# Kernel tuning notes

Hardware: AMD Instinct MI355X
Metric: run time of the kernel (lower is better)

Reference implementation:

```python
import jax, jax.numpy as jnp
import numpy as np

ENDING = False  # ending=False -> 'outgoing' triangle update; True -> 'incoming'
EPS = 1e-5


def _ln(x, w, b):
    m = jnp.mean(x, axis=-1, keepdims=True)
    v = jnp.mean((x - m) ** 2, axis=-1, keepdims=True)
    return (x - m) * jax.lax.rsqrt(v + EPS) * w + b


def setup_inputs() -> dict:
    key = jax.random.key(0)
    ks = jax.random.split(key, 6)
    B, N, D = 1, 384, 128
    s = 0.02
    return {
        "x": jax.random.normal(ks[0], (B, N, N, D), jnp.float32),
        "norm_in_w": jnp.ones((D,), jnp.float32),
        "norm_in_b": jnp.zeros((D,), jnp.float32),
        "w_g_in": jax.random.normal(ks[1], (2 * D, D), jnp.float32) * s,
        "w_p_in": jax.random.normal(ks[2], (2 * D, D), jnp.float32) * s,
        "w_g_out": jax.random.normal(ks[3], (D, D), jnp.float32) * s,
        "norm_out_w": jnp.ones((D,), jnp.float32),
        "norm_out_b": jnp.zeros((D,), jnp.float32),
        "w_p_out": jax.random.normal(ks[4], (D, D), jnp.float32) * s,
    }


def reference(x, norm_in_w, norm_in_b, w_g_in, w_p_in, w_g_out,
              norm_out_w, norm_out_b, w_p_out):
    D = x.shape[-1]
    xn = _ln(x, norm_in_w, norm_in_b)                       # [B,N,N,D]
    g_in = jax.nn.sigmoid(jnp.einsum('bijd,ed->bije', xn, w_g_in))  # [B,N,N,2D]
    p = jnp.einsum('bijd,ed->bije', xn, w_p_in) * g_in      # [B,N,N,2D]
    a, b = p[..., :D], p[..., D:]
    if ENDING:
        # incoming: out[i,j,d] = sum_k a[k,i,d] * b[k,j,d]
        t = jnp.einsum('bkid,bkjd->bijd', a, b)
    else:
        # outgoing: out[i,j,d] = sum_k a[i,k,d] * b[j,k,d]
        t = jnp.einsum('bikd,bjkd->bijd', a, b)
    g_out = jax.nn.sigmoid(jnp.einsum('bijd,ed->bije', xn, w_g_out))  # [B,N,N,D]
    return g_out * jnp.einsum('bijd,ed->bije', _ln(t, norm_out_w, norm_out_b), w_p_out)
```

## Files before the change

kernel.cpp:

```cpp
#include <hip/hip_runtime.h>
#include <hip/hip_bf16.h>
#include <math.h>

#define NPOS 147456
#define NSEQ 384

typedef __attribute__((ext_vector_type(4))) float f32x4;
typedef __attribute__((ext_vector_type(8))) short bf16x8;
typedef __attribute__((ext_vector_type(4))) short s16x4;

__device__ __forceinline__ unsigned short f2bf(float f){
  union { float f; unsigned u; } v; v.f = f;
  unsigned r = v.u + 0x7FFFu + ((v.u >> 16) & 1u);
  return (unsigned short)(r >> 16);
}
__device__ __forceinline__ float bf2f(unsigned short h){
  union { unsigned u; float f; } v; v.u = ((unsigned)h) << 16;
  return v.f;
}
__device__ __forceinline__ float fastsig(float x){
  return __builtin_amdgcn_rcpf(1.0f + __expf(-x));
}
__device__ __forceinline__ unsigned pk2(float lo, float hi){
  return (unsigned)f2bf(lo) | ((unsigned)f2bf(hi) << 16);
}
__device__ __forceinline__ void gl16(const unsigned short* g, unsigned short* l){
  __builtin_amdgcn_global_load_lds(
      (const __attribute__((address_space(1))) void*)g,
      (__attribute__((address_space(3))) void*)l, 16, 0, 0);
}

__global__ void wswz_all(const float* __restrict__ wgi, const float* __restrict__ wpi,
                         const float* __restrict__ wgo, const float* __restrict__ wpo,
                         unsigned short* __restrict__ wgi_s, unsigned short* __restrict__ wpi_s,
                         unsigned short* __restrict__ wgo_s, unsigned short* __restrict__ wpo_s){
  int i = blockIdx.x * 256 + threadIdx.x;
  int t = i >> 11;
  int r = i & 2047;
  const float* src; unsigned short* dst; int lt;
  if (t < 16)      { src = wgi; dst = wgi_s; lt = t;      }
  else if (t < 32) { src = wpi; dst = wpi_s; lt = t - 16; }
  else if (t < 40) { src = wgo; dst = wgo_s; lt = t - 32; }
  else             { src = wpo; dst = wpo_s; lt = t - 40; }
  int j = r & 7, lane = (r >> 3) & 63, kk = (r >> 9) & 3;
  int lrow = lane & 15, khh = lane >> 4;
  dst[lt*2048 + r] = f2bf(src[(lt*16 + lrow)*128 + kk*32 + khh*8 + j]);
}

__global__ __launch_bounds__(256, 4) void k1_ln_proj(
    const float* __restrict__ x,
    const float* __restrict__ ln_w, const float* __restrict__ ln_b,
    const unsigned short* __restrict__ wg_sw,
    const unsigned short* __restrict__ wp_sw,
    const unsigned short* __restrict__ wgo_sw,
    unsigned short* __restrict__ a_t,
    unsigned short* __restrict__ b_t,
    unsigned short* __restrict__ g_t)
{
  __shared__ unsigned short xn[128][128];
  unsigned short* wbuf = &xn[0][0];
  unsigned short* obuf = wbuf + 8192;

  const int tid  = threadIdx.x;
  const int posb = blockIdx.x * 128;
  const int lane = tid & 63;
  const int wid  = tid >> 6;

  const int rql = tid >> 2;
  const int q   = tid & 3;
  #pragma unroll
  for (int rr = 0; rr < 2; ++rr){
    int row = rr*64 + rql;
    const float* xr = x + (size_t)(posb + row) * 128 + q * 32;
    float v[32]; float s = 0.f, s2 = 0.f;
    #pragma unroll
    for (int j2 = 0; j2 < 8; ++j2){
      f32x4 t4 = *(const f32x4*)(xr + j2*4);
      #pragma unroll
      for (int m = 0; m < 4; ++m){ float f = t4[m]; v[j2*4+m] = f; s += f; s2 += f*f; }
    }
    s  += __shfl_xor(s, 1);  s  += __shfl_xor(s, 2);
    s2 += __shfl_xor(s2, 1); s2 += __shfl_xor(s2, 2);
    float mean = s * (1.f/128.f);
    float rstd = rsqrtf(s2 * (1.f/128.f) - mean*mean + 1e-5f);
    int sw = (row & 7) * 8;
    #pragma unroll
    for (int c = 0; c < 4; ++c){
      float n[8];
      #pragma unroll
      for (int j2 = 0; j2 < 8; ++j2){
        int k = q*32 + c*8 + j2;
        n[j2] = (v[c*8+j2] - mean) * rstd * ln_w[k] + ln_b[k];
      }
      uint4 u;
      u.x = pk2(n[0], n[1]); u.y = pk2(n[2], n[3]);
      u.z = pk2(n[4], n[5]); u.w = pk2(n[6], n[7]);
      *(uint4*)&xn[row][(q*32 + c*8) ^ sw] = u;
    }
  }
  __syncthreads();

  const int lrow = lane & 15, kh = lane >> 4;
  bf16x8 afrag[2][4];
  #pragma unroll
  for (int r = 0; r < 2; ++r){
    int row = wid*32 + r*16 + lrow;
    int sw = (row & 7) * 8;
    #pragma unroll
    for (int kk = 0; kk < 4; ++kk)
      afrag[r][kk] = *(const bf16x8*)&xn[row][(kk*32 + kh*8) ^ sw];
  }
  __syncthreads();

  const int kh4 = kh * 4;
  const int scl = wid*4 + kh;
  const int spo = lrow * 8;
  const int wl8 = wid*512 + lane*8;

#define STAGE_PAIR(et, b) do { \
    gl16(wg_sw + (size_t)(et)*2048 + wl8, wbuf + (2*(b)+0)*2048 + wid*512); \
    gl16(wp_sw + (size_t)(et)*2048 + wl8, wbuf + (2*(b)+1)*2048 + wid*512); \
  } while(0)
#define STAGE_G(et, b) do { \
    gl16(wgo_sw + (size_t)(et)*2048 + wl8, wbuf + (b)*2048 + wid*512); \
  } while(0)

  STAGE_PAIR(0, 0);
  __syncthreads();

  for (int et = 0; et < 16; ++et){
    const int b = et & 1;
    const unsigned short* wG = wbuf + (2*b+0)*2048 + lane*8;
    const unsigned short* wP = wbuf + (2*b+1)*2048 + lane*8;
    f32x4 accg0 = {0.f,0.f,0.f,0.f}, accg1 = {0.f,0.f,0.f,0.f};
    f32x4 accp0 = {0.f,0.f,0.f,0.f}, accp1 = {0.f,0.f,0.f,0.f};
    #pragma unroll
    for (int kk = 0; kk < 4; ++kk){
      bf16x8 G = *(const bf16x8*)(wG + kk*512);
      bf16x8 P = *(const bf16x8*)(wP + kk*512);
      accg0 = __builtin_amdgcn_mfma_f32_16x16x32_bf16(afrag[0][kk], G, accg0, 0, 0, 0);
      accg1 = __builtin_amdgcn_mfma_f32_16x16x32_bf16(afrag[1][kk], G, accg1, 0, 0, 0);
      accp0 = __builtin_amdgcn_mfma_f32_16x16x32_bf16(afrag[0][kk], P, accp0, 0, 0, 0);
      accp1 = __builtin_amdgcn_mfma_f32_16x16x32_bf16(afrag[1][kk], P, accp1, 0, 0, 0);
    }
    {
      uint2 u0, u1;
      u0.x = pk2(fastsig(accg0[0])*accp0[0], fastsig(accg0[1])*accp0[1]);
      u0.y = pk2(fastsig(accg0[2])*accp0[2], fastsig(accg0[3])*accp0[3]);
      u1.x = pk2(fastsig(accg1[0])*accp1[0], fastsig(accg1[1])*accp1[1]);
      u1.y = pk2(fastsig(accg1[2])*accp1[2], fastsig(accg1[3])*accp1[3]);
      *(uint2*)&obuf[b*2176 + lrow*136 + wid*32 + kh4]      = u0;
      *(uint2*)&obuf[b*2176 + lrow*136 + wid*32 + 16 + kh4] = u1;
    }
    if (et < 15) STAGE_PAIR(et+1, b^1);
    else         STAGE_G(0, 0);
    __syncthreads();
    {
      bf16x8 vv = *(const bf16x8*)&obuf[b*2176 + scl*136 + spo];
      int colg = et*16 + scl;
      unsigned short* dst = (et < 8) ? (a_t + (size_t)colg * NPOS)
                                     : (b_t + (size_t)(colg - 128) * NPOS);
      *(bf16x8*)(dst + posb + spo) = vv;
    }
  }

  for (int gt = 0; gt < 8; ++gt){
    const int b = gt & 1;
    const unsigned short* wQ = wbuf + b*2048 + lane*8;
    f32x4 a0 = {0.f,0.f,0.f,0.f}, a1 = {0.f,0.f,0.f,0.f};
    #pragma unroll
    for (int kk = 0; kk < 4; ++kk){
      bf16x8 Q = *(const bf16x8*)(wQ + kk*512);
      a0 = __builtin_amdgcn_mfma_f32_16x16x32_bf16(afrag[0][kk], Q, a0, 0, 0, 0);
      a1 = __builtin_amdgcn_mfma_f32_16x16x32_bf16(afrag[1][kk], Q, a1, 0, 0, 0);
    }
    {
      uint2 u0, u1;
      u0.x = pk2(fastsig(a0[0]), fastsig(a0[1]));
      u0.y = pk2(fastsig(a0[2]), fastsig(a0[3]));
      u1.x = pk2(fastsig(a1[0]), fastsig(a1[1]));
      u1.y = pk2(fastsig(a1[2]), fastsig(a1[3]));
      *(uint2*)&obuf[b*2176 + lrow*136 + wid*32 + kh4]      = u0;
      *(uint2*)&obuf[b*2176 + lrow*136 + wid*32 + 16 + kh4] = u1;
    }
    if (gt < 7) STAGE_G(gt+1, b^1);
    __syncthreads();
    {
      bf16x8 vv = *(const bf16x8*)&obuf[b*2176 + scl*136 + spo];
      *(bf16x8*)(g_t + (size_t)(gt*16 + scl) * NPOS + posb + spo) = vv;
    }
  }
#undef STAGE_PAIR
#undef STAGE_G
}

#define K2PAD 56
__global__ __launch_bounds__(256) void k2_tri(
    const unsigned short* __restrict__ a_t,
    const unsigned short* __restrict__ b_t,
    unsigned short* __restrict__ t_t)
{
  __shared__ unsigned short As[128][K2PAD];
  __shared__ unsigned short Bs[128][K2PAD];

  const int d  = blockIdx.z;
  const int i0 = blockIdx.y * 128;
  const int j0 = blockIdx.x * 128;
  const unsigned short* Ab = a_t + (size_t)d * NPOS;
  const unsigned short* Bb = b_t + (size_t)d * NPOS;

  const int tid = threadIdx.x;
  const int wid = tid >> 6, lane = tid & 63;
  const int wr = wid >> 1, wc = wid & 1;
  const int lrow = lane & 15, kh = (lane >> 4) * 8;

  f32x4 acc[4][4];
  #pragma unroll
  for (int r = 0; r < 4; ++r)
    #pragma unroll
    for (int c = 0; c < 4; ++c)
      acc[r][c] = (f32x4){0.f,0.f,0.f,0.f};

  const int sr = tid >> 1, sc = (tid & 1) * 16;

  for (int k0 = 0; k0 < NSEQ; k0 += 32){
    bf16x8 va0 = *(const bf16x8*)(Ab + (size_t)(i0 + sr) * NSEQ + k0 + sc);
    bf16x8 va1 = *(const bf16x8*)(Ab + (size_t)(i0 + sr) * NSEQ + k0 + sc + 8);
    bf16x8 vb0 = *(const bf16x8*)(Bb + (size_t)(j0 + sr) * NSEQ + k0 + sc);
    bf16x8 vb1 = *(const bf16x8*)(Bb + (size_t)(j0 + sr) * NSEQ + k0 + sc + 8);
    __syncthreads();
    *(bf16x8*)&As[sr][sc]     = va0;
    *(bf16x8*)&As[sr][sc + 8] = va1;
    *(bf16x8*)&Bs[sr][sc]     = vb0;
    *(bf16x8*)&Bs[sr][sc + 8] = vb1;
    __syncthreads();

    bf16x8 af[4], bfr[4];
    #pragma unroll
    for (int r = 0; r < 4; ++r)
      af[r] = *(const bf16x8*)&As[wr*64 + r*16 + lrow][kh];
    #pragma unroll
    for (int c = 0; c < 4; ++c)
      bfr[c] = *(const bf16x8*)&Bs[wc*64 + c*16 + lrow][kh];
    #pragma unroll
    for (int r = 0; r < 4; ++r)
      #pragma unroll
      for (int c = 0; c < 4; ++c)
        acc[r][c] = __builtin_amdgcn_mfma_f32_16x16x32_bf16(af[r], bfr[c], acc[r][c], 0, 0, 0);
  }

  unsigned short* Tb = t_t + (size_t)d * NPOS;
  #pragma unroll
  for (int r = 0; r < 4; ++r){
    int i = i0 + wr*64 + r*16 + (lane >> 4) * 4;
    #pragma unroll
    for (int c = 0; c < 4; ++c){
      int j = j0 + wc*64 + c*16 + lrow;
      #pragma unroll
      for (int jj = 0; jj < 4; ++jj)
        Tb[(size_t)(i + jj) * NSEQ + j] = f2bf(acc[r][c][jj]);
    }
  }
}

#define LNS 136
__global__ __launch_bounds__(256, 3) void k3_out(
    const unsigned short* __restrict__ t_t,
    const unsigned short* __restrict__ g_t,
    const float* __restrict__ ln_w, const float* __restrict__ ln_b,
    const unsigned short* __restrict__ wpo_sw,
    float* __restrict__ out)
{
  __shared__ unsigned short traw[128][136];
  __shared__ float regB[9024];
  __shared__ float smean[128], srs[128];

  const int tid = threadIdx.x;
  const int p0  = blockIdx.x * 128;
  const int lane = tid & 63, wid = tid >> 6;

  float* pps = regB;
  float* ppq = regB + 2048;
  unsigned short* lnt = (unsigned short*)regB;
  float (*ltile)[68] = (float(*)[68])regB;

  {
    int d = tid >> 1, c0 = (tid & 1) * 64;
    const unsigned short* src = t_t + (size_t)d * NPOS + p0 + c0;
    #pragma unroll
    for (int j = 0; j < 8; ++j)
      *(bf16x8*)&traw[d][c0 + j*8] = *(const bf16x8*)(src + j*8);
  }
  __syncthreads();

  const int pg = tid & 15, dh = tid >> 4;
  {
    float s8[8] = {0,0,0,0,0,0,0,0}, q8[8] = {0,0,0,0,0,0,0,0};
    #pragma unroll
    for (int jd = 0; jd < 8; ++jd){
      bf16x8 v = *(const bf16x8*)&traw[dh*8 + jd][pg*8];
      #pragma unroll
      for (int p = 0; p < 8; ++p){
        float f = bf2f((unsigned short)v[p]);
        s8[p] += f; q8[p] += f*f;
      }
    }
    #pragma unroll
    for (int p = 0; p < 8; ++p){
      pps[dh*128 + pg*8 + p] = s8[p];
      ppq[dh*128 + pg*8 + p] = q8[p];
    }
  }
  __syncthreads();
  if (tid < 128){
    float s = 0.f, q = 0.f;
    #pragma unroll
    for (int k = 0; k < 16; ++k){ s += pps[k*128 + tid]; q += ppq[k*128 + tid]; }
    float m = s * (1.f/128.f);
    smean[tid] = m;
    srs[tid]   = rsqrtf(q * (1.f/128.f) - m*m + 1e-5f);
  }
  __syncthreads();

  {
    float vv[8][8];
    #pragma unroll
    for (int jd = 0; jd < 8; ++jd){
      bf16x8 v = *(const bf16x8*)&traw[dh*8 + jd][pg*8];
      float w = ln_w[dh*8 + jd], bb = ln_b[dh*8 + jd];
      #pragma unroll
      for (int p = 0; p < 8; ++p)
        vv[jd][p] = (bf2f((unsigned short)v[p]) - smean[pg*8+p]) * srs[pg*8+p] * w + bb;
    }
    #pragma unroll
    for (int p = 0; p < 8; ++p){
      uint4 u;
      u.x = pk2(vv[0][p], vv[1][p]); u.y = pk2(vv[2][p], vv[3][p]);
      u.z = pk2(vv[4][p], vv[5][p]); u.w = pk2(vv[6][p], vv[7][p]);
      *(uint4*)&lnt[(size_t)(pg*8 + p)*LNS + dh*8] = u;
    }
  }
  __syncthreads();

  const int lrow = lane & 15, kh = (lane >> 4) * 8;
  bf16x8 af[2][4];
  #pragma unroll
  for (int r = 0; r < 2; ++r)
    #pragma unroll
    for (int kk = 0; kk < 4; ++kk)
      af[r][kk] = *(const bf16x8*)&lnt[(size_t)(wid*32 + r*16 + lrow)*LNS + kk*32 + kh];
  __syncthreads();

  {
    int e = tid >> 1, c0 = (tid & 1) * 64;
    const unsigned short* src = g_t + (size_t)e * NPOS + p0 + c0;
    #pragma unroll
    for (int j = 0; j < 8; ++j)
      *(bf16x8*)&traw[e][c0 + j*8] = *(const bf16x8*)(src + j*8);
  }
  __syncthreads();

  #pragma unroll
  for (int half = 0; half < 2; ++half){
    #pragma unroll
    for (int cf4 = 0; cf4 < 4; ++cf4){
      int cf = half*4 + cf4;
      const unsigned short* wq = wpo_sw + (size_t)cf*2048 + lane*8;
      bf16x8 bfr[4];
      #pragma unroll
      for (int kk = 0; kk < 4; ++kk)
        bfr[kk] = *(const bf16x8*)(wq + kk*512);
      f32x4 a0 = {0.f,0.f,0.f,0.f}, a1 = {0.f,0.f,0.f,0.f};
      #pragma unroll
      for (int kk = 0; kk < 4; ++kk){
        a0 = __builtin_amdgcn_mfma_f32_16x16x32_bf16(af[0][kk], bfr[kk], a0, 0, 0, 0);
        a1 = __builtin_amdgcn_mfma_f32_16x16x32_bf16(af[1][kk], bfr[kk], a1, 0, 0, 0);
      }
      int e = cf*16 + lrow;
      #pragma unroll
      for (int r = 0; r < 2; ++r){
        f32x4 av = r ? a1 : a0;
        int prow = wid*32 + r*16 + (lane >> 4)*4;
        #pragma unroll
        for (int jj = 0; jj < 4; ++jj){
          float g = bf2f(traw[e][prow + jj]);
          ltile[prow + jj][cf4*16 + lrow] = g * av[jj];
        }
      }
    }
    __syncthreads();
    {
      int pos = tid >> 1, he = tid & 1;
      const float* srcp = &ltile[pos][he*32];
      float* dst = out + (size_t)(p0 + pos)*128 + half*64 + he*32;
      #pragma unroll
      for (int j = 0; j < 8; ++j)
        *(f32x4*)(dst + j*4) = *(const f32x4*)(srcp + j*4);
    }
    __syncthreads();
  }
}

extern "C" void kernel_launch(void* const* d_in, const int* in_sizes, int n_in,
                              void* d_out, int out_size, void* d_ws, size_t ws_size,
                              hipStream_t stream) {
  (void)in_sizes; (void)n_in; (void)out_size; (void)ws_size;
  const float* x   = (const float*)d_in[0];
  const float* niw = (const float*)d_in[1];
  const float* nib = (const float*)d_in[2];
  const float* wgi = (const float*)d_in[3];
  const float* wpi = (const float*)d_in[4];
  const float* wgo = (const float*)d_in[5];
  const float* now = (const float*)d_in[6];
  const float* nob = (const float*)d_in[7];
  const float* wpo = (const float*)d_in[8];
  float* out = (float*)d_out;

  unsigned short* a_t   = (unsigned short*)d_ws;
  unsigned short* b_t   = a_t + (size_t)128 * NPOS;
  unsigned short* g_t   = b_t + (size_t)128 * NPOS;
  unsigned short* t_t   = g_t + (size_t)128 * NPOS;
  unsigned short* wgi_s = t_t + (size_t)128 * NPOS;
  unsigned short* wpi_s = wgi_s + 256 * 128;
  unsigned short* wgo_s = wpi_s + 256 * 128;
  unsigned short* wpo_s = wgo_s + 128 * 128;

  wswz_all<<<384, 256, 0, stream>>>(wgi, wpi, wgo, wpo, wgi_s, wpi_s, wgo_s, wpo_s);

  k1_ln_proj<<<NPOS/128, 256, 0, stream>>>(x, niw, nib, wgi_s, wpi_s, wgo_s, a_t, b_t, g_t);

  dim3 g2(3, 3, 128);
  k2_tri<<<g2, 256, 0, stream>>>(a_t, b_t, t_t);

  k3_out<<<NPOS/128, 256, 0, stream>>>(t_t, g_t, now, nob, wpo_s, out);
}
```

Baseline: 169.0 us.

## Load projection weights directly from global memory and use per-wave output staging

Drops the LDS double-buffered weight staging (global_load_lds) and its block-wide barriers in the projection kernel. Weight fragments are now read straight from global/L2 by each wave, and each wave transposes its own output tile in a private LDS region, so no __syncthreads is needed per tile. This removes 24 block barriers per block at the cost of redundant per-wave global weight reads that rely on cache hits. The within-wave LDS write-then-read relies on wave-level ordering without an explicit barrier.

```diff
diff --git a/kernel.cpp b/kernel.cpp
--- a/kernel.cpp
+++ b/kernel.cpp
@@ -23,11 +23,6 @@
 }
 __device__ __forceinline__ unsigned pk2(float lo, float hi){
   return (unsigned)f2bf(lo) | ((unsigned)f2bf(hi) << 16);
-}
-__device__ __forceinline__ void gl16(const unsigned short* g, unsigned short* l){
-  __builtin_amdgcn_global_load_lds(
-      (const __attribute__((address_space(1))) void*)g,
-      (__attribute__((address_space(3))) void*)l, 16, 0, 0);
 }
 
 __global__ void wswz_all(const float* __restrict__ wgi, const float* __restrict__ wpi,
@@ -58,8 +53,7 @@
     unsigned short* __restrict__ g_t)
 {
   __shared__ unsigned short xn[128][128];
-  unsigned short* wbuf = &xn[0][0];
-  unsigned short* obuf = wbuf + 8192;
+  unsigned short* obase = &xn[0][0];
 
   const int tid  = threadIdx.x;
   const int posb = blockIdx.x * 128;
@@ -112,26 +106,15 @@
   }
   __syncthreads();
 
+  unsigned short* ob = obase + wid * 640;
   const int kh4 = kh * 4;
-  const int scl = wid*4 + kh;
-  const int spo = lrow * 8;
-  const int wl8 = wid*512 + lane*8;
-
-#define STAGE_PAIR(et, b) do { \
-    gl16(wg_sw + (size_t)(et)*2048 + wl8, wbuf + (2*(b)+0)*2048 + wid*512); \
-    gl16(wp_sw + (size_t)(et)*2048 + wl8, wbuf + (2*(b)+1)*2048 + wid*512); \
-  } while(0)
-#define STAGE_G(et, b) do { \
-    gl16(wgo_sw + (size_t)(et)*2048 + wl8, wbuf + (b)*2048 + wid*512); \
-  } while(0)
-
-  STAGE_PAIR(0, 0);
-  __syncthreads();
+  const int och = lane >> 2;
+  const int opo = (lane & 3) * 8;
+  const size_t posw = (size_t)posb + wid*32;
 
   for (int et = 0; et < 16; ++et){
-    const int b = et & 1;
-    const unsigned short* wG = wbuf + (2*b+0)*2048 + lane*8;
-    const unsigned short* wP = wbuf + (2*b+1)*2048 + lane*8;
+    const unsigned short* wG = wg_sw + (size_t)et*2048 + lane*8;
+    const unsigned short* wP = wp_sw + (size_t)et*2048 + lane*8;
     f32x4 accg0 = {0.f,0.f,0.f,0.f}, accg1 = {0.f,0.f,0.f,0.f};
     f32x4 accp0 = {0.f,0.f,0.f,0.f}, accp1 = {0.f,0.f,0.f,0.f};
     #pragma unroll
@@ -149,24 +132,20 @@
       u0.y = pk2(fastsig(accg0[2])*accp0[2], fastsig(accg0[3])*accp0[3]);
       u1.x = pk2(fastsig(accg1[0])*accp1[0], fastsig(accg1[1])*accp1[1]);
       u1.y = pk2(fastsig(accg1[2])*accp1[2], fastsig(accg1[3])*accp1[3]);
-      *(uint2*)&obuf[b*2176 + lrow*136 + wid*32 + kh4]      = u0;
-      *(uint2*)&obuf[b*2176 + lrow*136 + wid*32 + 16 + kh4] = u1;
-    }
-    if (et < 15) STAGE_PAIR(et+1, b^1);
-    else         STAGE_G(0, 0);
-    __syncthreads();
+      *(uint2*)&ob[lrow*40 + kh4]      = u0;
+      *(uint2*)&ob[lrow*40 + 16 + kh4] = u1;
+    }
     {
-      bf16x8 vv = *(const bf16x8*)&obuf[b*2176 + scl*136 + spo];
-      int colg = et*16 + scl;
+      bf16x8 vv = *(const bf16x8*)&ob[och*40 + opo];
+      int colg = et*16 + och;
       unsigned short* dst = (et < 8) ? (a_t + (size_t)colg * NPOS)
                                      : (b_t + (size_t)(colg - 128) * NPOS);
-      *(bf16x8*)(dst + posb + spo) = vv;
+      *(bf16x8*)(dst + posw + opo) = vv;
     }
   }
 
   for (int gt = 0; gt < 8; ++gt){
-    const int b = gt & 1;
-    const unsigned short* wQ = wbuf + b*2048 + lane*8;
+    const unsigned short* wQ = wgo_sw + (size_t)gt*2048 + lane*8;
     f32x4 a0 = {0.f,0.f,0.f,0.f}, a1 = {0.f,0.f,0.f,0.f};
     #pragma unroll
     for (int kk = 0; kk < 4; ++kk){
@@ -180,18 +159,14 @@
       u0.y = pk2(fastsig(a0[2]), fastsig(a0[3]));
       u1.x = pk2(fastsig(a1[0]), fastsig(a1[1]));
       u1.y = pk2(fastsig(a1[2]), fastsig(a1[3]));
-      *(uint2*)&obuf[b*2176 + lrow*136 + wid*32 + kh4]      = u0;
-      *(uint2*)&obuf[b*2176 + lrow*136 + wid*32 + 16 + kh4] = u1;
-    }
-    if (gt < 7) STAGE_G(gt+1, b^1);
-    __syncthreads();
+      *(uint2*)&ob[lrow*40 + kh4]      = u0;
+      *(uint2*)&ob[lrow*40 + 16 + kh4] = u1;
+    }
     {
-      bf16x8 vv = *(const bf16x8*)&obuf[b*2176 + scl*136 + spo];
-      *(bf16x8*)(g_t + (size_t)(gt*16 + scl) * NPOS + posb + spo) = vv;
-    }
-  }
-#undef STAGE_PAIR
-#undef STAGE_G
+      bf16x8 vv = *(const bf16x8*)&ob[och*40 + opo];
+      *(bf16x8*)(g_t + (size_t)(gt*16 + och) * NPOS + posw + opo) = vv;
+    }
+  }
 }
 
 #define K2PAD 56
```

After: 176.9 us. +4.7%, slower.
